# Performance work log

Hardware: AMD Instinct MI355X
Metric: run time of the kernel (lower is better)

The kernel has to match this reference:

```python
import jax, jax.numpy as jnp
import numpy as np

B, S, H, F, K = 32, 512, 256, 256, 3
NBINS, MAX_MEL = 256, 2048


def _conv1d(x, w, b):
    # x: [B,S,Cin], w: [K,Cin,Cout] -> [B,S,Cout], padding 1 (SAME, k=3)
    return jax.lax.conv_general_dilated(x, w, (1,), 'SAME',
        dimension_numbers=('NWC', 'WIO', 'NWC')) + b


def _ln(x, g, b):
    m = jnp.mean(x, -1, keepdims=True)
    v = jnp.var(x, -1, keepdims=True)
    return (x - m) * jax.lax.rsqrt(v + 1e-5) * g + b


def _predictor(x, mask, p):
    # FastSpeech2 VariancePredictor (eval mode, dropout off)
    w1, b1, g1, be1, w2, b2, g2, be2, wl, bl = p
    h = _ln(jax.nn.relu(_conv1d(x, w1, b1)), g1, be1)
    h = _ln(jax.nn.relu(_conv1d(h, w2, b2)), g2, be2)
    out = (h @ wl + bl)[..., 0]  # [B,S]
    return jnp.where(mask, 0.0, out)  # masked_fill(mask, 0.0)


def _make_predictor_params(key, out_bias):
    ks = jax.random.split(key, 3)
    w1 = jax.random.normal(ks[0], (K, H, F), jnp.float32) * 0.03
    w2 = jax.random.normal(ks[1], (K, F, F), jnp.float32) * 0.03
    wl = jax.random.normal(ks[2], (F, 1), jnp.float32) * 0.02
    return [w1, jnp.zeros((F,), jnp.float32), jnp.ones((F,), jnp.float32), jnp.zeros((F,), jnp.float32),
            w2, jnp.zeros((F,), jnp.float32), jnp.ones((F,), jnp.float32), jnp.zeros((F,), jnp.float32),
            wl, jnp.full((1,), out_bias, jnp.float32)]


PNAMES = ['w1', 'b1', 'g1', 'be1', 'w2', 'b2', 'g2', 'be2', 'wl', 'bl']


def setup_inputs() -> dict:
    key = jax.random.key(0)
    ks = jax.random.split(key, 8)
    inp = {
        'x': jax.random.normal(ks[0], (B, S, H), jnp.float32),
        'src_mask': jnp.zeros((B, S), jnp.bool_),  # True = padded position
        'pitch_control': jnp.float32(1.0),
        'energy_control': jnp.float32(1.0),
        'duration_control': jnp.float32(1.0),
        'pitch_bins': jnp.linspace(-4.0, 4.0, NBINS - 1, dtype=jnp.float32),
        'energy_bins': jnp.linspace(-4.0, 4.0, NBINS - 1, dtype=jnp.float32),
        'pitch_emb': jax.random.normal(ks[1], (NBINS, H), jnp.float32) * 0.02,
        'energy_emb': jax.random.normal(ks[2], (NBINS, H), jnp.float32) * 0.02,
    }
    # duration predictor output bias 1.6 ~ log(5) -> avg ~4 frames/phoneme
    for i, (pref, ob) in enumerate([('dur', 1.6), ('pit', 0.0), ('ene', 0.0)]):
        for n, v in zip(PNAMES, _make_predictor_params(ks[3 + i], ob)):
            inp[pref + '_' + n] = v
    return inp


def reference(x, src_mask, pitch_control, energy_control, duration_control,
              pitch_bins, energy_bins, pitch_emb, energy_emb,
              dur_w1, dur_b1, dur_g1, dur_be1, dur_w2, dur_b2, dur_g2, dur_be2, dur_wl, dur_bl,
              pit_w1, pit_b1, pit_g1, pit_be1, pit_w2, pit_b2, pit_g2, pit_be2, pit_wl, pit_bl,
              ene_w1, ene_b1, ene_g1, ene_be1, ene_w2, ene_b2, ene_g2, ene_be2, ene_wl, ene_bl):
    dur_p = [dur_w1, dur_b1, dur_g1, dur_be1, dur_w2, dur_b2, dur_g2, dur_be2, dur_wl, dur_bl]
    pit_p = [pit_w1, pit_b1, pit_g1, pit_be1, pit_w2, pit_b2, pit_g2, pit_be2, pit_wl, pit_bl]
    ene_p = [ene_w1, ene_b1, ene_g1, ene_be1, ene_w2, ene_b2, ene_g2, ene_be2, ene_wl, ene_bl]

    log_dur = _predictor(x, src_mask, dur_p)                      # [B,S]
    pitch_pred = _predictor(x, src_mask, pit_p) * pitch_control   # inference: scaled prediction
    # torch.bucketize(v, bins) (right=False) == searchsorted side='left'
    x = x + pitch_emb[jnp.searchsorted(pitch_bins, pitch_pred, side='left')]
    energy_pred = _predictor(x, src_mask, ene_p) * energy_control
    x = x + energy_emb[jnp.searchsorted(energy_bins, energy_pred, side='left')]

    dur = jnp.maximum(jnp.round(jnp.exp(log_dur) - 1.0) * duration_control, 0.0)  # [B,S]
    dur_i = dur.astype(jnp.int32)
    mel_len = jnp.minimum(jnp.sum(dur_i, -1), MAX_MEL)            # [B]
    # Length regulator: frame t maps to phoneme idx = #{cumdur <= t}
    cum = jnp.cumsum(dur_i, 1)                                    # [B,S]
    t = jnp.arange(MAX_MEL, dtype=jnp.int32)
    idx = jax.vmap(lambda c: jnp.searchsorted(c, t, side='right'))(cum)  # [B,MAX_MEL]
    idx = jnp.clip(idx, 0, S - 1)
    x_exp = jnp.take_along_axis(x, idx[:, :, None], axis=1)       # [B,MAX_MEL,H]
    mel_mask = t[None, :] >= mel_len[:, None]                     # True = padded frame
    x_exp = jnp.where(mel_mask[:, :, None], 0.0, x_exp)
    return (x_exp, pitch_pred, energy_pred, log_dur, dur, mel_len, mel_mask)
```

## Files before the change

kernel.cpp:

```cpp
#include <hip/hip_runtime.h>
#include <stdint.h>

#define BB 32
#define SS 512
#define HH 256
#define MM (BB*SS)
#define MAXMEL 2048

typedef _Float16 f16;
typedef _Float16 f16x4 __attribute__((ext_vector_type(4)));
typedef _Float16 f16x8 __attribute__((ext_vector_type(8)));
typedef float    f32x16 __attribute__((ext_vector_type(16)));

#define BAR()  asm volatile("s_barrier" ::: "memory")
#define VMW9() asm volatile("s_waitcnt vmcnt(9)" ::: "memory")
#define VMW0() asm volatile("s_waitcnt vmcnt(0)" ::: "memory")

__device__ __forceinline__ size_t xoff8(int pane, int row) {
  return ((size_t)pane * MM + row) * 8;
}

#define AOFF  49152
#define ABUF  12352
#define AZ    61440
#define BBUF  24576
#define LDSSZ 73856
#define WSZP ((size_t)393216)

template<int NS, int RAW>
__global__ __launch_bounds__(256) void conv16(
    const f16* __restrict__ X0h, const f16* __restrict__ X0l,
    const f16* __restrict__ X1h_, const f16* __restrict__ X1l_,
    const f16* __restrict__ W0, const f16* __restrict__ W1,
    const float* __restrict__ bias0, const float* __restrict__ bias1,
    f16* __restrict__ Y0h, f16* __restrict__ Y0l,
    f16* __restrict__ Y1h, f16* __restrict__ Y1l,
    float* __restrict__ Craw)
{
  __shared__ __align__(16) unsigned char smem[LDSSZ];
  const int tid = threadIdx.x;
  const int lane = tid & 63, wid = tid >> 6;
  const int bm = blockIdx.x, bn = blockIdx.y, bz = blockIdx.z;
  const int l31 = lane & 31, half = lane >> 5;
  const int wr = wid >> 1, wc = wid & 1;

  const int s0 = RAW ? bz * 8 : 0;
  const f16* Xh = (RAW || bz == 0) ? X0h : X1h_;
  const f16* Xl = (RAW || bz == 0) ? X0l : X1l_;
  const f16* Wp = (RAW || bz == 0) ? W0 : W1;

  const f16* sb[9]; int sdst[9]; int sdb[9]; size_t sstr[9];
  #pragma unroll
  for (int i = 0; i < 9; ++i) {
    int j = wid * 9 + i;
    if (j < 12) {
      int p = j / 6, rem = j % 6, g = rem / 3, seg = rem % 3;
      int lr = seg * 64 + lane;
      int row = bm * 128 - 32 + lr;
      row = row < 0 ? 0 : (row >= MM ? MM - 1 : row);
      sb[i]   = (p ? Xl : Xh) + ((size_t)g * MM + row) * 8;
      sstr[i] = (size_t)MM * 16;
      sdst[i] = AOFF + p * 6144 + g * 3072 + lr * 16;
      sdb[i]  = ABUF;
    } else {
      int jj = j - 12;
      int p = jj / 12, rest = jj % 12;
      int tap = rest >> 2, q = rest & 3;
      int g = q >> 1, h2 = q & 1;
      sb[i]   = Wp + ((((((size_t)(bn * 16) * 2 + p) * 3 + tap) * 2 + g) * 128)
                      + h2 * 64 + lane) * 8;
      sstr[i] = 12288;
      sdst[i] = p * 12288 + tap * 4096 + g * 2048 + h2 * 1024 + lane * 16;
      sdb[i]  = BBUF;
    }
  }

  int a_addr[3][2][2];
  #pragma unroll
  for (int tap = 0; tap < 3; ++tap)
    #pragma unroll
    for (int mi = 0; mi < 2; ++mi) {
      int row_l = wr * 64 + mi * 32 + l31;
      int sseq = (bm & 3) * 128 + row_l + tap - 1;
      bool valid = (unsigned)sseq < 512u;
      int lr = row_l + tap + 31;
      #pragma unroll
      for (int p = 0; p < 2; ++p)
        a_addr[tap][mi][p] = valid ? (AOFF + p * 6144 + half * 3072 + lr * 16)
                                   : AZ;
    }
  int b_base[2];
  #pragma unroll
  for (int n = 0; n < 2; ++n)
    b_base[n] = half * 2048 + (wc * 64 + n * 32 + l31) * 16;

  f32x16 acc[2][2];
  #pragma unroll
  for (int mi = 0; mi < 2; ++mi)
    #pragma unroll
    for (int ni = 0; ni < 2; ++ni) acc[mi][ni] = (f32x16)0.f;

  auto STAGE = [&](int buf, int step) {
    #pragma unroll
    for (int i = 0; i < 9; ++i)
      __builtin_amdgcn_global_load_lds(
        (const __attribute__((address_space(1))) void*)(sb[i] + (size_t)step * sstr[i]),
        (__attribute__((address_space(3))) void*)(smem + sdst[i] + buf * sdb[i]),
        16, 0, 0);
  };

  auto COMP = [&](int buf) {
    #pragma unroll
    for (int tap = 0; tap < 3; ++tap) {
      f16x8 av[2][2], bv[2][2];
      #pragma unroll
      for (int p = 0; p < 2; ++p)
        #pragma unroll
        for (int q = 0; q < 2; ++q) {
          av[p][q] = *(const f16x8*)(smem + (a_addr[tap][q][p] + buf * ABUF));
          bv[p][q] = *(const f16x8*)(smem + (buf * BBUF + p * 12288 + tap * 4096 + b_base[q]));
        }
      #pragma unroll
      for (int mi = 0; mi < 2; ++mi)
        #pragma unroll
        for (int ni = 0; ni < 2; ++ni) {
          acc[mi][ni] = __builtin_amdgcn_mfma_f32_32x32x16_f16(av[0][mi], bv[0][ni], acc[mi][ni], 0, 0, 0);
          acc[mi][ni] = __builtin_amdgcn_mfma_f32_32x32x16_f16(av[0][mi], bv[1][ni], acc[mi][ni], 0, 0, 0);
          acc[mi][ni] = __builtin_amdgcn_mfma_f32_32x32x16_f16(av[1][mi], bv[0][ni], acc[mi][ni], 0, 0, 0);
        }
    }
  };

  if (tid < 4) {
    *(float4*)(smem + AZ + tid * 16) = make_float4(0.f, 0.f, 0.f, 0.f);
    *(float4*)(smem + AZ + ABUF + tid * 16) = make_float4(0.f, 0.f, 0.f, 0.f);
  }
  STAGE(0, s0); STAGE(1, s0 + 1);
  __syncthreads();

  #pragma unroll
  for (int i = 0; i < NS; ++i) {
    COMP(i & 1);
    BAR();
    if (i < NS - 2)       { STAGE(i & 1, s0 + i + 2); VMW9(); }
    else if (i == NS - 2) { VMW0(); }
    BAR();
  }

  if constexpr (RAW) {
    float* C = Craw + (size_t)bz * MM * 256;
    #pragma unroll
    for (int mi = 0; mi < 2; ++mi)
      #pragma unroll
      for (int ni = 0; ni < 2; ++ni) {
        int colg = bn * 128 + wc * 64 + ni * 32 + l31;
        #pragma unroll
        for (int r = 0; r < 16; ++r) {
          int rowl = (r & 3) + 8 * (r >> 2) + 4 * half;
          size_t rowg = (size_t)bm * 128 + wr * 64 + mi * 32 + rowl;
          C[rowg * 256 + colg] = acc[mi][ni][r];
        }
      }
  } else {
    const float* bias = bz ? bias1 : bias0;
    f16* Yh = bz ? Y1h : Y0h;
    f16* Yl = bz ? Y1l : Y0l;
    #pragma unroll
    for (int mi = 0; mi < 2; ++mi)
      #pragma unroll
      for (int ni = 0; ni < 2; ++ni) {
        int colg = bn * 128 + wc * 64 + ni * 32 + l31;
        float bvs = bias[colg];
        size_t cbase = (size_t)(colg >> 3) * MM * 8 + (colg & 7);
        #pragma unroll
        for (int r = 0; r < 16; ++r) {
          int rowl = (r & 3) + 8 * (r >> 2) + 4 * half;
          int rowg = bm * 128 + wr * 64 + mi * 32 + rowl;
          float v = fmaxf(acc[mi][ni][r] + bvs, 0.f);
          f16 h = (f16)v;
          f16 l = (f16)(v - (float)h);
          size_t o = cbase + (size_t)rowg * 8;
          Yh[o] = h;
          Yl[o] = l;
        }
      }
  }
}

__global__ __launch_bounds__(256) void wsplit6(
    const float* __restrict__ W0, const float* __restrict__ W1,
    const float* __restrict__ W2, const float* __restrict__ W3,
    const float* __restrict__ W4, const float* __restrict__ W5,
    f16* __restrict__ Wt)
{
  int z = blockIdx.y;
  const float* W = z==0?W0 : z==1?W1 : z==2?W2 : z==3?W3 : z==4?W4 : W5;
  f16* T = Wt + (size_t)z * WSZP;
  int id = blockIdx.x * 256 + threadIdx.x;
  int col = id & 127;
  int t = id >> 7;
  int g = t & 1; t >>= 1;
  int tap = t % 3; t /= 3;
  int p = t & 1; t >>= 1;
  int s = t & 15;
  int bn = t >> 4;
  int chan = s * 16 + g * 8;
  int colg = bn * 128 + col;
  f16x8 o;
  #pragma unroll
  for (int e = 0; e < 8; ++e) {
    float w = W[(size_t)(tap * 256 + chan + e) * 256 + colg];
    f16 h = (f16)w;
    o[e] = p ? (f16)(w - (float)h) : h;
  }
  *(f16x8*)(T + (size_t)id * 8) = o;
}

__global__ __launch_bounds__(256) void split2(
    const float* __restrict__ X, f16* __restrict__ Hi, f16* __restrict__ Lo)
{
  int id = blockIdx.x * 256 + threadIdx.x;
  int row = id >> 5, pane = id & 31;
  const float* src = X + (size_t)row * 256 + pane * 8;
  float4 v0 = *(const float4*)src;
  float4 v1 = *(const float4*)(src + 4);
  float vv[8] = {v0.x, v0.y, v0.z, v0.w, v1.x, v1.y, v1.z, v1.w};
  f16x8 h, l;
  #pragma unroll
  for (int j = 0; j < 8; ++j) {
    f16 hh = (f16)vv[j];
    h[j] = hh;
    l[j] = (f16)(vv[j] - (float)hh);
  }
  size_t o = xoff8(pane, row);
  *(f16x8*)(Hi + o) = h;
  *(f16x8*)(Lo + o) = l;
}


__global__ __launch_bounds__(256) void lnF(
    f16* __restrict__ P0h, f16* __restrict__ P0l,
    f16* __restrict__ P1h, f16* __restrict__ P1l,
    const float* __restrict__ g0, const float* __restrict__ be0,
    const float* __restrict__ g1, const float* __restrict__ be1)
{
  int z = blockIdx.y;
  f16* Ph = z ? P1h : P0h;
  f16* Pl = z ? P1l : P0l;
  const float* g  = z ? g1 : g0;
  const float* be = z ? be1 : be0;
  int tid = threadIdx.x, lane = tid & 63;
  int row  = blockIdx.x * 8 + (tid >> 6) * 2 + (lane >> 5);
  int pane = lane & 31;
  size_t o = xoff8(pane, row);
  f16x8 h = *(const f16x8*)(Ph + o);
  f16x8 l = *(const f16x8*)(Pl + o);
  float v[8];
  #pragma unroll
  for (int j = 0; j < 8; ++j) v[j] = (float)h[j] + (float)l[j];
  float s = 0.f, q = 0.f;
  #pragma unroll
  for (int j = 0; j < 8; ++j) { s += v[j]; q += v[j] * v[j]; }
  #pragma unroll
  for (int d = 16; d > 0; d >>= 1) { s += __shfl_xor(s, d); q += __shfl_xor(q, d); }
  float mean = s * (1.f / 256.f);
  float var  = q * (1.f / 256.f) - mean * mean;
  float inv  = 1.0f / sqrtf(var + 1e-5f);
  float4 ga = *(const float4*)(g + pane * 8);
  float4 gb = *(const float4*)(g + pane * 8 + 4);
  float4 ba = *(const float4*)(be + pane * 8);
  float4 bb = *(const float4*)(be + pane * 8 + 4);
  float gv[8] = {ga.x, ga.y, ga.z, ga.w, gb.x, gb.y, gb.z, gb.w};
  float bv[8] = {ba.x, ba.y, ba.z, ba.w, bb.x, bb.y, bb.z, bb.w};
  #pragma unroll
  for (int j = 0; j < 8; ++j) {
    float oo = (v[j] - mean) * inv * gv[j] + bv[j];
    f16 hh = (f16)oo;
    h[j] = hh;
    l[j] = (f16)(oo - (float)hh);
  }
  *(f16x8*)(Ph + o) = h;
  *(f16x8*)(Pl + o) = l;
}

__global__ __launch_bounds__(256) void lnheadD(
    const f16* __restrict__ U0h, const f16* __restrict__ U0l,
    const f16* __restrict__ U1h, const f16* __restrict__ U1l,
    const float* __restrict__ g0, const float* __restrict__ be0,
    const float* __restrict__ wl0, const float* __restrict__ bl0,
    const float* __restrict__ g1, const float* __restrict__ be1,
    const float* __restrict__ wl1, const float* __restrict__ bl1,
    const unsigned char* __restrict__ mask, const float* __restrict__ pc,
    float* __restrict__ o_ldur, float* __restrict__ pred_d,
    float* __restrict__ o_pit,
    const float* __restrict__ pbins, const float* __restrict__ pemb,
    const f16* __restrict__ XPh, const f16* __restrict__ XPl,
    f16* __restrict__ X1h, f16* __restrict__ X1l)
{
  int z = blockIdx.y;
  int tid = threadIdx.x, lane = tid & 63;
  int row  = blockIdx.x * 8 + (tid >> 6) * 2 + (lane >> 5);
  int pane = lane & 31;
  size_t o = xoff8(pane, row);
  const f16* Uh = z ? U1h : U0h;
  const f16* Ul = z ? U1l : U0l;
  f16x8 h = *(const f16x8*)(Uh + o);
  f16x8 l = *(const f16x8*)(Ul + o);
  float v[8];
  #pragma unroll
  for (int j = 0; j < 8; ++j) v[j] = (float)h[j] + (float)l[j];
  float s = 0.f, q = 0.f;
  #pragma unroll
  for (int j = 0; j < 8; ++j) { s += v[j]; q += v[j] * v[j]; }
  #pragma unroll
  for (int d = 16; d > 0; d >>= 1) { s += __shfl_xor(s, d); q += __shfl_xor(q, d); }
  float mean = s * (1.f / 256.f);
  float var  = q * (1.f / 256.f) - mean * mean;
  float inv  = 1.0f / sqrtf(var + 1e-5f);
  const float* g  = z ? g1  : g0;
  const float* be = z ? be1 : be0;
  const float* wl = z ? wl1 : wl0;
  float4 ga = *(const float4*)(g + pane * 8);
  float4 gb = *(const float4*)(g + pane * 8 + 4);
  float4 ba = *(const float4*)(be + pane * 8);
  float4 bb = *(const float4*)(be + pane * 8 + 4);
  float4 wa = *(const float4*)(wl + pane * 8);
  float4 wb = *(const float4*)(wl + pane * 8 + 4);
  float gv[8] = {ga.x, ga.y, ga.z, ga.w, gb.x, gb.y, gb.z, gb.w};
  float bv[8] = {ba.x, ba.y, ba.z, ba.w, bb.x, bb.y, bb.z, bb.w};
  float wv[8] = {wa.x, wa.y, wa.z, wa.w, wb.x, wb.y, wb.z, wb.w};
  float acc = 0.f;
  #pragma unroll
  for (int j = 0; j < 8; ++j)
    acc += ((v[j] - mean) * inv * gv[j] + bv[j]) * wv[j];
  #pragma unroll
  for (int d = 16; d > 0; d >>= 1) acc += __shfl_xor(acc, d);
  float r = acc + (z ? bl1 : bl0)[0];
  if (mask[row]) r = 0.f;
  if (z == 0) {
    if (pane == 0) { o_ldur[row] = r; pred_d[row] = r; }
  } else {
    r *= pc[0];
    if (pane == 0) o_pit[row] = r;
    int lo = 0, hi = 255;
    while (lo < hi) { int mid = (lo + hi) >> 1; if (pbins[mid] < r) lo = mid + 1; else hi = mid; }
    f16x8 xh = *(const f16x8*)(XPh + o);
    f16x8 xl = *(const f16x8*)(XPl + o);
    float4 ea = *(const float4*)(pemb + (size_t)lo * HH + pane * 8);
    float4 eb = *(const float4*)(pemb + (size_t)lo * HH + pane * 8 + 4);
    float ev[8] = {ea.x, ea.y, ea.z, ea.w, eb.x, eb.y, eb.z, eb.w};
    #pragma unroll
    for (int j = 0; j < 8; ++j) {
      float oo = (float)xh[j] + (float)xl[j] + ev[j];
      f16 hh = (f16)oo;
      xh[j] = hh;
      xl[j] = (f16)(oo - (float)hh);
    }
    *(f16x8*)(X1h + o) = xh;
    *(f16x8*)(X1l + o) = xl;
  }
}

__global__ __launch_bounds__(256) void lnS(
    const float* __restrict__ C0, const float* __restrict__ C1,
    const float* __restrict__ bias,
    const float* __restrict__ g, const float* __restrict__ be,
    f16* __restrict__ Yh, f16* __restrict__ Yl)
{
  int tid = threadIdx.x, lane = tid & 63;
  int row  = blockIdx.x * 8 + (tid >> 6) * 2 + (lane >> 5);
  int pane = lane & 31;
  size_t ci = (size_t)row * 256 + pane * 8;
  float4 a0 = *(const float4*)(C0 + ci);
  float4 a1 = *(const float4*)(C0 + ci + 4);
  float4 b0 = *(const float4*)(C1 + ci);
  float4 b1 = *(const float4*)(C1 + ci + 4);
  float4 s0 = *(const float4*)(bias + pane * 8);
  float4 s1 = *(const float4*)(bias + pane * 8 + 4);
  float v[8] = {fmaxf(a0.x + b0.x + s0.x, 0.f), fmaxf(a0.y + b0.y + s0.y, 0.f),
                fmaxf(a0.z + b0.z + s0.z, 0.f), fmaxf(a0.w + b0.w + s0.w, 0.f),
                fmaxf(a1.x + b1.x + s1.x, 0.f), fmaxf(a1.y + b1.y + s1.y, 0.f),
                fmaxf(a1.z + b1.z + s1.z, 0.f), fmaxf(a1.w + b1.w + s1.w, 0.f)};
  float s = 0.f, q = 0.f;
  #pragma unroll
  for (int j = 0; j < 8; ++j) { s += v[j]; q += v[j] * v[j]; }
  #pragma unroll
  for (int d = 16; d > 0; d >>= 1) { s += __shfl_xor(s, d); q += __shfl_xor(q, d); }
  float mean = s * (1.f / 256.f);
  float var  = q * (1.f / 256.f) - mean * mean;
  float inv  = 1.0f / sqrtf(var + 1e-5f);
  float4 ga = *(const float4*)(g + pane * 8);
  float4 gb = *(const float4*)(g + pane * 8 + 4);
  float4 ba = *(const float4*)(be + pane * 8);
  float4 bb = *(const float4*)(be + pane * 8 + 4);
  float gv[8] = {ga.x, ga.y, ga.z, ga.w, gb.x, gb.y, gb.z, gb.w};
  float bv[8] = {ba.x, ba.y, ba.z, ba.w, bb.x, bb.y, bb.z, bb.w};
  f16x8 h, l;
  #pragma unroll
  for (int j = 0; j < 8; ++j) {
    float oo = (v[j] - mean) * inv * gv[j] + bv[j];
    f16 hh = (f16)oo;
    h[j] = hh;
    l[j] = (f16)(oo - (float)hh);
  }
  size_t o = xoff8(pane, row);
  *(f16x8*)(Yh + o) = h;
  *(f16x8*)(Yl + o) = l;
}

__global__ __launch_bounds__(256) void lnheadS(
    const float* __restrict__ C0, const float* __restrict__ C1,
    const float* __restrict__ bias,
    const float* __restrict__ g, const float* __restrict__ be,
    const float* __restrict__ wl, const float* __restrict__ bl,
    const unsigned char* __restrict__ mask, const float* __restrict__ ec,
    float* __restrict__ o_ene,
    const float* __restrict__ ebins, const float* __restrict__ eemb,
    const f16* __restrict__ X1h, const f16* __restrict__ X1l,
    f16* __restrict__ X2h, f16* __restrict__ X2l)
{
  int tid = threadIdx.x, lane = tid & 63;
  int row  = blockIdx.x * 8 + (tid >> 6) * 2 + (lane >> 5);
  int pane = lane & 31;
  size_t ci = (size_t)row * 256 + pane * 8;
  float4 a0 = *(const float4*)(C0 + ci);
  float4 a1 = *(const float4*)(C0 + ci + 4);
  float4 b0 = *(const float4*)(C1 + ci);
  float4 b1 = *(const float4*)(C1 + ci + 4);
  float4 s0 = *(const float4*)(bias + pane * 8);
  float4 s1 = *(const float4*)(bias + pane * 8 + 4);
  float v[8] = {fmaxf(a0.x + b0.x + s0.x, 0.f), fmaxf(a0.y + b0.y + s0.y, 0.f),
                fmaxf(a0.z + b0.z + s0.z, 0.f), fmaxf(a0.w + b0.w + s0.w, 0.f),
                fmaxf(a1.x + b1.x + s1.x, 0.f), fmaxf(a1.y + b1.y + s1.y, 0.f),
                fmaxf(a1.z + b1.z + s1.z, 0.f), fmaxf(a1.w + b1.w + s1.w, 0.f)};
  float s = 0.f, q = 0.f;
  #pragma unroll
  for (int j = 0; j < 8; ++j) { s += v[j]; q += v[j] * v[j]; }
  #pragma unroll
  for (int d = 16; d > 0; d >>= 1) { s += __shfl_xor(s, d); q += __shfl_xor(q, d); }
  float mean = s * (1.f / 256.f);
  float var  = q * (1.f / 256.f) - mean * mean;
  float inv  = 1.0f / sqrtf(var + 1e-5f);
  float4 ga = *(const float4*)(g + pane * 8);
  float4 gb = *(const float4*)(g + pane * 8 + 4);
  float4 ba = *(const float4*)(be + pane * 8);
  float4 bb = *(const float4*)(be + pane * 8 + 4);
  float4 wa = *(const float4*)(wl + pane * 8);
  float4 wb = *(const float4*)(wl + pane * 8 + 4);
  float gv[8] = {ga.x, ga.y, ga.z, ga.w, gb.x, gb.y, gb.z, gb.w};
  float bv[8] = {ba.x, ba.y, ba.z, ba.w, bb.x, bb.y, bb.z, bb.w};
  float wv[8] = {wa.x, wa.y, wa.z, wa.w, wb.x, wb.y, wb.z, wb.w};
  float acc = 0.f;
  #pragma unroll
  for (int j = 0; j < 8; ++j)
    acc += ((v[j] - mean) * inv * gv[j] + bv[j]) * wv[j];
  #pragma unroll
  for (int d = 16; d > 0; d >>= 1) acc += __shfl_xor(acc, d);
  float r = acc + bl[0];
  if (mask[row]) r = 0.f;
  r *= ec[0];
  if (pane == 0) o_ene[row] = r;
  int lo = 0, hi = 255;
  while (lo < hi) { int mid = (lo + hi) >> 1; if (ebins[mid] < r) lo = mid + 1; else hi = mid; }
  size_t o = xoff8(pane, row);
  f16x8 xh = *(const f16x8*)(X1h + o);
  f16x8 xl = *(const f16x8*)(X1l + o);
  float4 ea = *(const float4*)(eemb + (size_t)lo * HH + pane * 8);
  float4 eb = *(const float4*)(eemb + (size_t)lo * HH + pane * 8 + 4);
  float ev[8] = {ea.x, ea.y, ea.z, ea.w, eb.x, eb.y, eb.z, eb.w};
  #pragma unroll
  for (int j = 0; j < 8; ++j) {
    float oo = (float)xh[j] + (float)xl[j] + ev[j];
    f16 hh = (f16)oo;
    xh[j] = hh;
    xl[j] = (f16)(oo - (float)hh);
  }
  *(f16x8*)(X2h + o) = xh;
  *(f16x8*)(X2l + o) = xl;
}

__global__ __launch_bounds__(512) void dur_post(
    const float* __restrict__ logdur, const float* __restrict__ dc,
    float* __restrict__ out_dur, float* __restrict__ out_mel_len,
    int* __restrict__ cum_ws, int* __restrict__ mel_len_ws)
{
  __shared__ int wsum[8];
  int b = blockIdx.x, t = threadIdx.x;
  float ld = logdur[b * SS + t];
  float d  = fmaxf(rintf(expf(ld) - 1.f) * dc[0], 0.f);
  out_dur[b * SS + t] = d;
  int di = (int)d;
  int lane = t & 63, w = t >> 6;
  int x = di;
  #pragma unroll
  for (int dd = 1; dd < 64; dd <<= 1) {
    int n = __shfl_up(x, dd);
    if (lane >= dd) x += n;
  }
  if (lane == 63) wsum[w] = x;
  __syncthreads();
  int off = 0;
  for (int i = 0; i < w; ++i) off += wsum[i];
  x += off;
  cum_ws[b * SS + t] = x;
  if (t == SS - 1) {
    int ml = min(x, MAXMEL);
    mel_len_ws[b] = ml;
    out_mel_len[b] = (float)ml;
  }
}

__global__ __launch_bounds__(256) void gather_planes(
    const f16* __restrict__ Xhi, const f16* __restrict__ Xlo,
    const int* __restrict__ cum, const int* __restrict__ mel_len_ws,
    float* __restrict__ out_x, float* __restrict__ out_mask)
{
  __shared__ int c[SS];
  int b   = blockIdx.y;
  int tid = threadIdx.x;
  c[tid]       = cum[b * SS + tid];
  c[tid + 256] = cum[b * SS + tid + 256];
  __syncthreads();
  int lane = tid & 63, w = tid >> 6;
  int t = blockIdx.x * 8 + w * 2 + (lane >> 5);
  int pane = lane & 31;
  int lo = 0, hi = SS;
  while (lo < hi) { int mid = (lo + hi) >> 1; if (c[mid] <= t) lo = mid + 1; else hi = mid; }
  int idx = min(lo, SS - 1);
  int ml  = mel_len_ws[b];
  bool m  = (t >= ml);
  float v[8] = {0.f, 0.f, 0.f, 0.f, 0.f, 0.f, 0.f, 0.f};
  if (!m) {
    size_t o = xoff8(pane, b * SS + idx);
    f16x8 xh = *(const f16x8*)(Xhi + o);
    f16x8 xl = *(const f16x8*)(Xlo + o);
    #pragma unroll
    for (int j = 0; j < 8; ++j) v[j] = (float)xh[j] + (float)xl[j];
  }
  float* dst = out_x + ((size_t)b * MAXMEL + t) * HH + pane * 8;
  *(float4*)dst       = make_float4(v[0], v[1], v[2], v[3]);
  *(float4*)(dst + 4) = make_float4(v[4], v[5], v[6], v[7]);
  if (pane == 0) out_mask[b * MAXMEL + t] = m ? 1.f : 0.f;
}

extern "C" void kernel_launch(void* const* d_in, const int* in_sizes, int n_in,
                              void* d_out, int out_size, void* d_ws, size_t ws_size,
                              hipStream_t stream) {
  const float* x     = (const float*)d_in[0];
  const unsigned char* smask = (const unsigned char*)d_in[1];
  const float* pc    = (const float*)d_in[2];
  const float* ec    = (const float*)d_in[3];
  const float* dc    = (const float*)d_in[4];
  const float* pbins = (const float*)d_in[5];
  const float* ebins = (const float*)d_in[6];
  const float* pemb  = (const float*)d_in[7];
  const float* eemb  = (const float*)d_in[8];

  float* out = (float*)d_out;
  float* o_xexp  = out;
  float* o_pit   = out + (size_t)16777216;
  float* o_ene   = o_pit + 16384;
  float* o_ldur  = o_ene + 16384;
  float* o_dur   = o_ldur + 16384;
  float* o_mlen  = o_dur + 16384;
  float* o_mmask = o_mlen + 32;

  const size_t PL = (size_t)MM * HH;
  f16* p = (f16*)d_ws;
  f16 *XPh = p,        *XPl = p + PL;
  f16 *Tdh = p + 2*PL, *Tdl = p + 3*PL;
  f16 *Tph = p + 4*PL, *Tpl = p + 5*PL;
  f16 *Udh = p + 6*PL, *Udl = p + 7*PL;
  f16 *Uph = p + 8*PL, *Upl = p + 9*PL;
  f16 *X1h = p + 10*PL, *X1l = p + 11*PL;
  f16 *Teh = p + 12*PL, *Tel = p + 13*PL;
  f16 *X2h = p + 14*PL, *X2l = p + 15*PL;
  f16* Wt  = p + 16*PL;
  float* C0 = (float*)(Wt + 6 * WSZP);
  float* C1 = C0 + (size_t)MM * 256;
  float* pred_d = C1 + (size_t)MM * 256;
  int*   cum = (int*)(pred_d + MM);
  int*   mlw = cum + MM;

  #define WPK(i) (Wt + (size_t)(i) * WSZP)

  wsplit6<<<dim3(192, 6), 256, 0, stream>>>(
      (const float*)d_in[9], (const float*)d_in[13], (const float*)d_in[19],
      (const float*)d_in[23], (const float*)d_in[29], (const float*)d_in[33], Wt);

  split2<<<2048, 256, 0, stream>>>(x, XPh, XPl);

  dim3 cgrid(128, 2, 2);
  dim3 rgrid8(MM / 8);
  dim3 rgrid8x2(MM / 8, 2);

  conv16<16, 0><<<cgrid, 256, 0, stream>>>(
      XPh, XPl, XPh, XPl, WPK(0), WPK(2),
      (const float*)d_in[10], (const float*)d_in[20],
      Tdh, Tdl, Tph, Tpl, nullptr);
  lnF<<<rgrid8x2, 256, 0, stream>>>(Tdh, Tdl, Tph, Tpl,
      (const float*)d_in[11], (const float*)d_in[12],
      (const float*)d_in[21], (const float*)d_in[22]);
  conv16<16, 0><<<cgrid, 256, 0, stream>>>(
      Tdh, Tdl, Tph, Tpl, WPK(1), WPK(3),
      (const float*)d_in[14], (const float*)d_in[24],
      Udh, Udl, Uph, Upl, nullptr);
  lnheadD<<<rgrid8x2, 256, 0, stream>>>(
      Udh, Udl, Uph, Upl,
      (const float*)d_in[15], (const float*)d_in[16],
      (const float*)d_in[17], (const float*)d_in[18],
      (const float*)d_in[25], (const float*)d_in[26],
      (const float*)d_in[27], (const float*)d_in[28],
      smask, pc, o_ldur, pred_d, o_pit, pbins, pemb,
      XPh, XPl, X1h, X1l);
  dur_post<<<BB, 512, 0, stream>>>(pred_d, dc, o_dur, o_mlen, cum, mlw);

  conv16<8, 1><<<cgrid, 256, 0, stream>>>(
      X1h, X1l, X1h, X1l, WPK(4), WPK(4),
      nullptr, nullptr, nullptr, nullptr, nullptr, nullptr, C0);
  lnS<<<rgrid8, 256, 0, stream>>>(C0, C1, (const float*)d_in[30],
      (const float*)d_in[31], (const float*)d_in[32], Teh, Tel);
  conv16<8, 1><<<cgrid, 256, 0, stream>>>(
      Teh, Tel, Teh, Tel, WPK(5), WPK(5),
      nullptr, nullptr, nullptr, nullptr, nullptr, nullptr, C0);
  lnheadS<<<rgrid8, 256, 0, stream>>>(C0, C1, (const float*)d_in[34],
      (const float*)d_in[35], (const float*)d_in[36],
      (const float*)d_in[37], (const float*)d_in[38],
      smask, ec, o_ene, ebins, eemb, X1h, X1l, X2h, X2l);

  dim3 ggrid(MAXMEL / 8, BB);
  gather_planes<<<ggrid, 256, 0, stream>>>(X2h, X2l, cum, mlw, o_xexp, o_mmask);

  #undef WPK
}
```

Baseline: 233.0 us.

## Switch conv GEMM to K=8 MFMA steps with a four-stage LDS pipeline

The split-fp16 conv kernel now consumes 8 input channels per step using the 32x32x8 f16 MFMA instead of 16 channels with 32x32x16. Each stage is half as large, which lets a four-buffer ring fit in LDS where there were two buffers before. The main loop drops one barrier per iteration and issues the prefetch three steps ahead. The weight repacking kernel is changed to match the new layout. The trade-off is twice as many loop iterations, a smaller MFMA shape, and 4-byte LDS reads, in exchange for deeper latency hiding of the global-to-LDS loads.

```diff
diff --git a/kernel.cpp b/kernel.cpp
--- a/kernel.cpp
+++ b/kernel.cpp
@@ -12,23 +12,26 @@
 typedef _Float16 f16x8 __attribute__((ext_vector_type(8)));
 typedef float    f32x16 __attribute__((ext_vector_type(16)));
 
-#define BAR()  asm volatile("s_barrier" ::: "memory")
-#define VMW9() asm volatile("s_waitcnt vmcnt(9)" ::: "memory")
-#define VMW0() asm volatile("s_waitcnt vmcnt(0)" ::: "memory")
+#define BAR()   asm volatile("s_barrier" ::: "memory")
+#define VMW10() asm volatile("s_waitcnt vmcnt(10)" ::: "memory")
+#define VMW5()  asm volatile("s_waitcnt vmcnt(5)"  ::: "memory")
+#define VMW0()  asm volatile("s_waitcnt vmcnt(0)"  ::: "memory")
+
+#define MFMA8(a,b,c) __builtin_amdgcn_mfma_f32_32x32x8f16(a,b,c,0,0,0)
 
 __device__ __forceinline__ size_t xoff8(int pane, int row) {
   return ((size_t)pane * MM + row) * 8;
 }
 
-#define AOFF  49152
-#define ABUF  12352
-#define AZ    61440
-#define BBUF  24576
-#define LDSSZ 73856
 #define WSZP ((size_t)393216)
 
+#define AZS   6160
+#define BOFF  24640
+#define BBS   12288
+#define LDSSZ 73792
+
 template<int NS, int RAW>
-__global__ __launch_bounds__(256) void conv16(
+__global__ __launch_bounds__(256) void conv8(
     const f16* __restrict__ X0h, const f16* __restrict__ X0l,
     const f16* __restrict__ X1h_, const f16* __restrict__ X1l_,
     const f16* __restrict__ W0, const f16* __restrict__ W1,
@@ -44,34 +47,34 @@
   const int l31 = lane & 31, half = lane >> 5;
   const int wr = wid >> 1, wc = wid & 1;
 
-  const int s0 = RAW ? bz * 8 : 0;
+  const int s0 = RAW ? bz * NS : 0;
   const f16* Xh = (RAW || bz == 0) ? X0h : X1h_;
   const f16* Xl = (RAW || bz == 0) ? X0l : X1l_;
   const f16* Wp = (RAW || bz == 0) ? W0 : W1;
 
-  const f16* sb[9]; int sdst[9]; int sdb[9]; size_t sstr[9];
-  #pragma unroll
-  for (int i = 0; i < 9; ++i) {
-    int j = wid * 9 + i;
-    if (j < 12) {
-      int p = j / 6, rem = j % 6, g = rem / 3, seg = rem % 3;
+  const f16* sb[5]; int sdst[5]; int sisA[5]; size_t sstr[5];
+  #pragma unroll
+  for (int i = 0; i < 5; ++i) {
+    int j = (wid < 2) ? (wid * 5 + i) : (10 + (wid - 2) * 4 + i);
+    if (j > 17) j = 17;
+    if (j < 6) {
+      int p = j / 3, seg = j % 3;
       int lr = seg * 64 + lane;
       int row = bm * 128 - 32 + lr;
       row = row < 0 ? 0 : (row >= MM ? MM - 1 : row);
-      sb[i]   = (p ? Xl : Xh) + ((size_t)g * MM + row) * 8;
-      sstr[i] = (size_t)MM * 16;
-      sdst[i] = AOFF + p * 6144 + g * 3072 + lr * 16;
-      sdb[i]  = ABUF;
+      sb[i]   = (p ? Xl : Xh) + (size_t)row * 8;
+      sstr[i] = (size_t)MM * 8;
+      sdst[i] = p * 3072 + seg * 1024 + lane * 16;
+      sisA[i] = 1;
     } else {
-      int jj = j - 12;
-      int p = jj / 12, rest = jj % 12;
-      int tap = rest >> 2, q = rest & 3;
-      int g = q >> 1, h2 = q & 1;
-      sb[i]   = Wp + ((((((size_t)(bn * 16) * 2 + p) * 3 + tap) * 2 + g) * 128)
-                      + h2 * 64 + lane) * 8;
-      sstr[i] = 12288;
-      sdst[i] = p * 12288 + tap * 4096 + g * 2048 + h2 * 1024 + lane * 16;
-      sdb[i]  = BBUF;
+      int jj = j - 6;
+      int p = jj / 6, rest = jj % 6;
+      int tap = rest >> 1, h = rest & 1;
+      sb[i]   = Wp + ((((((size_t)bn * 32) * 2 + p) * 3 + tap) * 2 + h) * 512)
+                   + lane * 8;
+      sstr[i] = 6144;
+      sdst[i] = (p * 3 + tap) * 2048 + h * 1024 + lane * 16;
+      sisA[i] = 0;
     }
   }
 
@@ -86,13 +89,12 @@
       int lr = row_l + tap + 31;
       #pragma unroll
       for (int p = 0; p < 2; ++p)
-        a_addr[tap][mi][p] = valid ? (AOFF + p * 6144 + half * 3072 + lr * 16)
-                                   : AZ;
+        a_addr[tap][mi][p] = valid ? (p * 3072 + lr * 16 + half * 8) : 6144;
     }
   int b_base[2];
   #pragma unroll
   for (int n = 0; n < 2; ++n)
-    b_base[n] = half * 2048 + (wc * 64 + n * 32 + l31) * 16;
+    b_base[n] = half * 1024 + (wc * 64 + n * 32 + l31) * 8;
 
   f32x16 acc[2][2];
   #pragma unroll
@@ -102,49 +104,48 @@
 
   auto STAGE = [&](int buf, int step) {
     #pragma unroll
-    for (int i = 0; i < 9; ++i)
+    for (int i = 0; i < 5; ++i) {
+      int dst = (sisA[i] ? (buf * AZS) : (BOFF + buf * BBS)) + sdst[i];
       __builtin_amdgcn_global_load_lds(
         (const __attribute__((address_space(1))) void*)(sb[i] + (size_t)step * sstr[i]),
-        (__attribute__((address_space(3))) void*)(smem + sdst[i] + buf * sdb[i]),
-        16, 0, 0);
+        (__attribute__((address_space(3))) void*)(smem + dst), 16, 0, 0);
+    }
   };
 
   auto COMP = [&](int buf) {
     #pragma unroll
     for (int tap = 0; tap < 3; ++tap) {
-      f16x8 av[2][2], bv[2][2];
+      f16x4 av[2][2], bv[2][2];
       #pragma unroll
       for (int p = 0; p < 2; ++p)
         #pragma unroll
         for (int q = 0; q < 2; ++q) {
-          av[p][q] = *(const f16x8*)(smem + (a_addr[tap][q][p] + buf * ABUF));
-          bv[p][q] = *(const f16x8*)(smem + (buf * BBUF + p * 12288 + tap * 4096 + b_base[q]));
+          av[p][q] = *(const f16x4*)(smem + (buf * AZS + a_addr[tap][q][p]));
+          bv[p][q] = *(const f16x4*)(smem + (BOFF + buf * BBS + p * 6144 + tap * 2048 + b_base[q]));
         }
       #pragma unroll
       for (int mi = 0; mi < 2; ++mi)
         #pragma unroll
         for (int ni = 0; ni < 2; ++ni) {
-          acc[mi][ni] = __builtin_amdgcn_mfma_f32_32x32x16_f16(av[0][mi], bv[0][ni], acc[mi][ni], 0, 0, 0);
-          acc[mi][ni] = __builtin_amdgcn_mfma_f32_32x32x16_f16(av[0][mi], bv[1][ni], acc[mi][ni], 0, 0, 0);
-          acc[mi][ni] = __builtin_amdgcn_mfma_f32_32x32x16_f16(av[1][mi], bv[0][ni], acc[mi][ni], 0, 0, 0);
+          acc[mi][ni] = MFMA8(av[0][mi], bv[0][ni], acc[mi][ni]);
+          acc[mi][ni] = MFMA8(av[0][mi], bv[1][ni], acc[mi][ni]);
+          acc[mi][ni] = MFMA8(av[1][mi], bv[0][ni], acc[mi][ni]);
         }
     }
   };
 
-  if (tid < 4) {
-    *(float4*)(smem + AZ + tid * 16) = make_float4(0.f, 0.f, 0.f, 0.f);
-    *(float4*)(smem + AZ + ABUF + tid * 16) = make_float4(0.f, 0.f, 0.f, 0.f);
-  }
-  STAGE(0, s0); STAGE(1, s0 + 1);
+  if (tid < 4)
+    *(float4*)(smem + tid * AZS + 6144) = make_float4(0.f, 0.f, 0.f, 0.f);
+  STAGE(0, s0); STAGE(1, s0 + 1); STAGE(2, s0 + 2);
   __syncthreads();
 
-  #pragma unroll
+  #pragma unroll 4
   for (int i = 0; i < NS; ++i) {
-    COMP(i & 1);
-    BAR();
-    if (i < NS - 2)       { STAGE(i & 1, s0 + i + 2); VMW9(); }
+    COMP(i & 3);
+    if (i + 3 < NS) { STAGE((i + 3) & 3, s0 + i + 3); VMW10(); }
+    else if (i == NS - 3) { VMW5(); }
     else if (i == NS - 2) { VMW0(); }
-    BAR();
+    if (i < NS - 1) BAR();
   }
 
   if constexpr (RAW) {
@@ -197,21 +198,23 @@
   const float* W = z==0?W0 : z==1?W1 : z==2?W2 : z==3?W3 : z==4?W4 : W5;
   f16* T = Wt + (size_t)z * WSZP;
   int id = blockIdx.x * 256 + threadIdx.x;
-  int col = id & 127;
-  int t = id >> 7;
-  int g = t & 1; t >>= 1;
-  int tap = t % 3; t /= 3;
-  int p = t & 1; t >>= 1;
-  int s = t & 15;
-  int bn = t >> 4;
-  int chan = s * 16 + g * 8;
-  int colg = bn * 128 + col;
+  int u = id & 63;
+  int r = id >> 6;
+  int h = r & 1; r >>= 1;
+  int tap = r % 3; r /= 3;
+  int p = r & 1; r >>= 1;
+  int s = r & 31;
+  int bn = r >> 5;
+  int chan = s * 8 + h * 4;
+  int col0 = bn * 128 + 2 * u;
   f16x8 o;
   #pragma unroll
-  for (int e = 0; e < 8; ++e) {
-    float w = W[(size_t)(tap * 256 + chan + e) * 256 + colg];
-    f16 h = (f16)w;
-    o[e] = p ? (f16)(w - (float)h) : h;
+  for (int e = 0; e < 4; ++e) {
+    float w0 = W[(size_t)(tap * 256 + chan + e) * 256 + col0];
+    float w1 = W[(size_t)(tap * 256 + chan + e) * 256 + col0 + 1];
+    f16 h0 = (f16)w0, h1 = (f16)w1;
+    o[e]     = p ? (f16)(w0 - (float)h0) : h0;
+    o[4 + e] = p ? (f16)(w1 - (float)h1) : h1;
   }
   *(f16x8*)(T + (size_t)id * 8) = o;
 }
@@ -594,14 +597,14 @@
   dim3 rgrid8(MM / 8);
   dim3 rgrid8x2(MM / 8, 2);
 
-  conv16<16, 0><<<cgrid, 256, 0, stream>>>(
+  conv8<32, 0><<<cgrid, 256, 0, stream>>>(
       XPh, XPl, XPh, XPl, WPK(0), WPK(2),
       (const float*)d_in[10], (const float*)d_in[20],
       Tdh, Tdl, Tph, Tpl, nullptr);
   lnF<<<rgrid8x2, 256, 0, stream>>>(Tdh, Tdl, Tph, Tpl,
       (const float*)d_in[11], (const float*)d_in[12],
       (const float*)d_in[21], (const float*)d_in[22]);
-  conv16<16, 0><<<cgrid, 256, 0, stream>>>(
+  conv8<32, 0><<<cgrid, 256, 0, stream>>>(
       Tdh, Tdl, Tph, Tpl, WPK(1), WPK(3),
       (const float*)d_in[14], (const float*)d_in[24],
       Udh, Udl, Uph, Upl, nullptr);
@@ -615,12 +618,12 @@
       XPh, XPl, X1h, X1l);
   dur_post<<<BB, 512, 0, stream>>>(pred_d, dc, o_dur, o_mlen, cum, mlw);
 
-  conv16<8, 1><<<cgrid, 256, 0, stream>>>(
+  conv8<16, 1><<<cgrid, 256, 0, stream>>>(
       X1h, X1l, X1h, X1l, WPK(4), WPK(4),
       nullptr, nullptr, nullptr, nullptr, nullptr, nullptr, C0);
   lnS<<<rgrid8, 256, 0, stream>>>(C0, C1, (const float*)d_in[30],
       (const float*)d_in[31], (const float*)d_in[32], Teh, Tel);
-  conv16<8, 1><<<cgrid, 256, 0, stream>>>(
+  conv8<16, 1><<<cgrid, 256, 0, stream>>>(
       Teh, Tel, Teh, Tel, WPK(5), WPK(5),
       nullptr, nullptr, nullptr, nullptr, nullptr, nullptr, C0);
   lnheadS<<<rgrid8, 256, 0, stream>>>(C0, C1, (const float*)d_in[34],
```

New measurement: 271.2 us. +16.4%, slower.

## Load conv activations directly from global memory instead of staging through LDS

Applied to the files above, without the earlier changes.

The activation (A) operand of the conv MFMA kernel is now read straight from global memory into registers for each tap, and the LDS staging buffers and zero-row padding for A are removed. Boundary rows are zeroed in registers using validity flags. LDS use drops to the weight double buffer only, and launch bounds request 3 blocks per CU to raise occupancy. The cost is that each A row is fetched three times (once per tap) from global or cache with no LDS reuse, and those loads now sit on the compute path rather than being prefetched.

```diff
diff --git a/kernel.cpp b/kernel.cpp
--- a/kernel.cpp
+++ b/kernel.cpp
@@ -13,22 +13,20 @@
 typedef float    f32x16 __attribute__((ext_vector_type(16)));
 
 #define BAR()  asm volatile("s_barrier" ::: "memory")
-#define VMW9() asm volatile("s_waitcnt vmcnt(9)" ::: "memory")
+#define VMW6() asm volatile("s_waitcnt vmcnt(6)" ::: "memory")
 #define VMW0() asm volatile("s_waitcnt vmcnt(0)" ::: "memory")
 
 __device__ __forceinline__ size_t xoff8(int pane, int row) {
   return ((size_t)pane * MM + row) * 8;
 }
 
-#define AOFF  49152
-#define ABUF  12352
-#define AZ    61440
+#define WSZP ((size_t)393216)
+
 #define BBUF  24576
-#define LDSSZ 73856
-#define WSZP ((size_t)393216)
+#define LDSSZ 49152
 
 template<int NS, int RAW>
-__global__ __launch_bounds__(256) void conv16(
+__global__ __launch_bounds__(256, 3) void conv16(
     const f16* __restrict__ X0h, const f16* __restrict__ X0l,
     const f16* __restrict__ X1h_, const f16* __restrict__ X1l_,
     const f16* __restrict__ W0, const f16* __restrict__ W1,
@@ -49,46 +47,33 @@
   const f16* Xl = (RAW || bz == 0) ? X0l : X1l_;
   const f16* Wp = (RAW || bz == 0) ? W0 : W1;
 
-  const f16* sb[9]; int sdst[9]; int sdb[9]; size_t sstr[9];
-  #pragma unroll
-  for (int i = 0; i < 9; ++i) {
-    int j = wid * 9 + i;
-    if (j < 12) {
-      int p = j / 6, rem = j % 6, g = rem / 3, seg = rem % 3;
-      int lr = seg * 64 + lane;
-      int row = bm * 128 - 32 + lr;
-      row = row < 0 ? 0 : (row >= MM ? MM - 1 : row);
-      sb[i]   = (p ? Xl : Xh) + ((size_t)g * MM + row) * 8;
-      sstr[i] = (size_t)MM * 16;
-      sdst[i] = AOFF + p * 6144 + g * 3072 + lr * 16;
-      sdb[i]  = ABUF;
-    } else {
-      int jj = j - 12;
-      int p = jj / 12, rest = jj % 12;
-      int tap = rest >> 2, q = rest & 3;
-      int g = q >> 1, h2 = q & 1;
-      sb[i]   = Wp + ((((((size_t)(bn * 16) * 2 + p) * 3 + tap) * 2 + g) * 128)
-                      + h2 * 64 + lane) * 8;
-      sstr[i] = 12288;
-      sdst[i] = p * 12288 + tap * 4096 + g * 2048 + h2 * 1024 + lane * 16;
-      sdb[i]  = BBUF;
-    }
-  }
-
-  int a_addr[3][2][2];
+  const f16* sb[6]; int sdst[6];
+  #pragma unroll
+  for (int i = 0; i < 6; ++i) {
+    int j = wid * 6 + i;
+    int p = j / 12, rest = j % 12;
+    int tap = rest >> 2, q = rest & 3;
+    int g = q >> 1, h2 = q & 1;
+    sb[i]   = Wp + ((((((size_t)(bn * 16) * 2 + p) * 3 + tap) * 2 + g) * 128)
+                    + h2 * 64 + lane) * 8;
+    sdst[i] = p * 12288 + tap * 4096 + g * 2048 + h2 * 1024 + lane * 16;
+  }
+
+  const f16* aptr[3][2][2];
   #pragma unroll
   for (int tap = 0; tap < 3; ++tap)
     #pragma unroll
     for (int mi = 0; mi < 2; ++mi) {
       int row_l = wr * 64 + mi * 32 + l31;
-      int sseq = (bm & 3) * 128 + row_l + tap - 1;
-      bool valid = (unsigned)sseq < 512u;
-      int lr = row_l + tap + 31;
-      #pragma unroll
-      for (int p = 0; p < 2; ++p)
-        a_addr[tap][mi][p] = valid ? (AOFF + p * 6144 + half * 3072 + lr * 16)
-                                   : AZ;
+      int rowg = bm * 128 + row_l + tap - 1;
+      rowg = rowg < 0 ? 0 : (rowg >= MM ? MM - 1 : rowg);
+      size_t o = ((size_t)half * MM + rowg) * 8;
+      aptr[tap][mi][0] = Xh + o;
+      aptr[tap][mi][1] = Xl + o;
     }
+  const bool vld00 = ((bm & 3) * 128 + (wr * 64 + l31) - 1) >= 0;
+  const bool vld12 = ((bm & 3) * 128 + (wr * 64 + 32 + l31) + 1) < 512;
+
   int b_base[2];
   #pragma unroll
   for (int n = 0; n < 2; ++n)
@@ -102,14 +87,15 @@
 
   auto STAGE = [&](int buf, int step) {
     #pragma unroll
-    for (int i = 0; i < 9; ++i)
+    for (int i = 0; i < 6; ++i)
       __builtin_amdgcn_global_load_lds(
-        (const __attribute__((address_space(1))) void*)(sb[i] + (size_t)step * sstr[i]),
-        (__attribute__((address_space(3))) void*)(smem + sdst[i] + buf * sdb[i]),
+        (const __attribute__((address_space(1))) void*)(sb[i] + (size_t)step * 12288),
+        (__attribute__((address_space(3))) void*)(smem + sdst[i] + buf * BBUF),
         16, 0, 0);
   };
 
-  auto COMP = [&](int buf) {
+  auto COMP = [&](int buf, int step) {
+    const size_t astp = (size_t)step * (MM * 16);
     #pragma unroll
     for (int tap = 0; tap < 3; ++tap) {
       f16x8 av[2][2], bv[2][2];
@@ -117,9 +103,11 @@
       for (int p = 0; p < 2; ++p)
         #pragma unroll
         for (int q = 0; q < 2; ++q) {
-          av[p][q] = *(const f16x8*)(smem + (a_addr[tap][q][p] + buf * ABUF));
+          av[p][q] = *(const f16x8*)(aptr[tap][q][p] + astp);
           bv[p][q] = *(const f16x8*)(smem + (buf * BBUF + p * 12288 + tap * 4096 + b_base[q]));
         }
+      if (tap == 0) { if (!vld00) { av[0][0] = (f16x8)(f16)0.f; av[1][0] = (f16x8)(f16)0.f; } }
+      if (tap == 2) { if (!vld12) { av[0][1] = (f16x8)(f16)0.f; av[1][1] = (f16x8)(f16)0.f; } }
       #pragma unroll
       for (int mi = 0; mi < 2; ++mi)
         #pragma unroll
@@ -131,18 +119,14 @@
     }
   };
 
-  if (tid < 4) {
-    *(float4*)(smem + AZ + tid * 16) = make_float4(0.f, 0.f, 0.f, 0.f);
-    *(float4*)(smem + AZ + ABUF + tid * 16) = make_float4(0.f, 0.f, 0.f, 0.f);
-  }
   STAGE(0, s0); STAGE(1, s0 + 1);
   __syncthreads();
 
   #pragma unroll
   for (int i = 0; i < NS; ++i) {
-    COMP(i & 1);
+    COMP(i & 1, s0 + i);
     BAR();
-    if (i < NS - 2)       { STAGE(i & 1, s0 + i + 2); VMW9(); }
+    if (i < NS - 2)       { STAGE(i & 1, s0 + i + 2); VMW6(); }
     else if (i == NS - 2) { VMW0(); }
     BAR();
   }
```

Measured after the change: 249.7 us. 1.07x slower.
